# Kernel tuning notes

Hardware: AMD Instinct MI355X
Metric: run time of the kernel (lower is better)

Reference implementation:

```python
import jax, jax.numpy as jnp
import numpy as np

H = 1024        # hidden_size
V = 50257       # output_size (vocab)
L = 2048        # max_length (encoder sequence)


def setup_inputs() -> dict:
    key = jax.random.key(0)
    ks = jax.random.split(key, 10)
    s = 1.0 / np.sqrt(H)
    return {
        "input_tok": jax.random.randint(ks[0], (1,), 0, V),
        "hidden": jax.random.normal(ks[1], (2, 1, H), dtype=jnp.float32),
        "encoder_hiddens": jax.random.normal(ks[2], (L, H), dtype=jnp.float32),
        # learned parameters
        "emb": jax.random.normal(ks[3], (V, H), dtype=jnp.float32),
        "W_ih": jax.random.uniform(ks[4], (2, H, H), jnp.float32, -s, s),   # per-direction input weights
        "W_hh": jax.random.uniform(ks[5], (2, H, H), jnp.float32, -s, s),   # per-direction recurrent weights
        "b_ih": jax.random.uniform(ks[6], (2, H), jnp.float32, -s, s),
        "b_hh": jax.random.uniform(ks[7], (2, H), jnp.float32, -s, s),
        "W_out": jax.random.uniform(ks[8], (V, 4 * H), jnp.float32, -s, s),
        "b_out": jax.random.uniform(ks[9], (V,), jnp.float32, -s, s),
    }


def reference(input_tok, hidden, encoder_hiddens, emb, W_ih, W_hh, b_ih, b_hh, W_out, b_out):
    # embedding lookup -> (H,)  (dropout is identity in eval mode)
    x = emb[input_tok[0]]
    # single-step bidirectional vanilla RNN cell (both directions see the same x):
    # h' = tanh(x W_ih^T + b_ih + h0 W_hh^T + b_hh), per direction d in {fwd, bwd}
    h0 = hidden[:, 0, :]                                    # (2, H)
    h = jnp.tanh(jnp.einsum('dho,o->dh', W_ih, x) + b_ih
                 + jnp.einsum('dho,do->dh', W_hh, h0) + b_hh)  # (2, H)
    # dot-product attention per direction over encoder states (L, H)
    energy = jnp.einsum('dh,lh->dl', h, encoder_hiddens)    # (2, L)
    attn = jax.nn.softmax(energy, axis=-1)                  # (2, L)
    attn_out = jnp.einsum('dl,lh->dh', attn, encoder_hiddens)  # (2, H)
    # concat: (attn_fwd, h_fwd, attn_bwd, h_bwd) -> (1, 4H)
    concat = jnp.concatenate([attn_out[0], h[0], attn_out[1], h[1]])[None, :]
    logits = concat @ W_out.T + b_out                       # (1, V)
    output = jax.nn.log_softmax(logits, axis=1)
    return output, h[:, None, :]                            # ((1, V), (2, 1, H))
```

## Files before the change

kernel.cpp:

```cpp
#include <hip/hip_runtime.h>
#include <cmath>

#define HDIM 1024
#define LSEQ 2048
#define VOCAB 50257
#define LOGIT_BLOCKS ((VOCAB + 3) / 4)

__device__ __forceinline__ float wave_sum(float v) {
#pragma unroll
    for (int off = 32; off; off >>= 1) v += __shfl_down(v, off, 64);
    return v;
}

__device__ __forceinline__ void lse_combine(float& m, float& s, float m2, float s2) {
    float nm = fmaxf(m, m2);
    s = s * expf(m - nm) + s2 * expf(m2 - nm);
    m = nm;
}

__global__ void rnn_kernel(const int* __restrict__ tok,
                           const float* __restrict__ hidden,
                           const float* __restrict__ emb,
                           const float* __restrict__ W_ih,
                           const float* __restrict__ W_hh,
                           const float* __restrict__ b_ih,
                           const float* __restrict__ b_hh,
                           float* __restrict__ concat,
                           float* __restrict__ out_h) {
    int wave = threadIdx.x >> 6, lane = threadIdx.x & 63;
    int row = blockIdx.x * 4 + wave;
    int d = row >> 10, i = row & 1023;
    int t = tok[0];
    const float* x  = emb + (size_t)t * HDIM;
    const float* h0 = hidden + d * HDIM;
    const float* wi = W_ih + (size_t)d * HDIM * HDIM + (size_t)i * HDIM;
    const float* wh = W_hh + (size_t)d * HDIM * HDIM + (size_t)i * HDIM;
    float acc = 0.f;
#pragma unroll
    for (int p = 0; p < 4; ++p) {
        int o = p * 256 + lane * 4;
        float4 a = *(const float4*)(wi + o);
        float4 b = *(const float4*)(x + o);
        acc += a.x * b.x + a.y * b.y + a.z * b.z + a.w * b.w;
        float4 c = *(const float4*)(wh + o);
        float4 e = *(const float4*)(h0 + o);
        acc += c.x * e.x + c.y * e.y + c.z * e.z + c.w * e.w;
    }
    acc = wave_sum(acc);
    if (lane == 0) {
        float hv = tanhf(acc + b_ih[d * HDIM + i] + b_hh[d * HDIM + i]);
        concat[d * 2048 + 1024 + i] = hv;
        out_h[d * HDIM + i] = hv;
    }
}

__global__ void flash_attn_kernel(const float* __restrict__ enc,
                                  const float* __restrict__ concat,
                                  float* __restrict__ part,
                                  float* __restrict__ pm_a,
                                  float* __restrict__ ps_a) {
    __shared__ float e_sh[32];
    int b = blockIdx.x;
    int d = b >> 6, c = b & 63;
    int t = threadIdx.x, wave = t >> 6, lane = t & 63;
    int base = c * 32;
    const float* h = concat + d * 2048 + 1024;

    for (int r = 0; r < 8; ++r) {
        int ll = wave * 8 + r;
        const float* er = enc + (size_t)(base + ll) * HDIM;
        float acc = 0.f;
#pragma unroll
        for (int p = 0; p < 4; ++p) {
            int o = p * 256 + lane * 4;
            float4 a = *(const float4*)(er + o);
            float4 bb = *(const float4*)(h + o);
            acc += a.x * bb.x + a.y * bb.y + a.z * bb.z + a.w * bb.w;
        }
        acc = wave_sum(acc);
        if (lane == 0) e_sh[ll] = acc;
    }
    __syncthreads();

    float m_c = -1e30f;
#pragma unroll
    for (int l = 0; l < 32; ++l) m_c = fmaxf(m_c, e_sh[l]);
    float s_c = 0.f;
    float acc0 = 0, acc1 = 0, acc2 = 0, acc3 = 0;
    for (int l = 0; l < 32; ++l) {
        float p = expf(e_sh[l] - m_c);
        s_c += p;
        const float* row = enc + (size_t)(base + l) * HDIM;
        acc0 += p * row[t];
        acc1 += p * row[t + 256];
        acc2 += p * row[t + 512];
        acc3 += p * row[t + 768];
    }
    float* pp = part + (size_t)b * HDIM;
    pp[t] = acc0; pp[t + 256] = acc1; pp[t + 512] = acc2; pp[t + 768] = acc3;
    if (t == 0) { pm_a[b] = m_c; ps_a[b] = s_c; }
}

__global__ void attn_combine_kernel(const float* __restrict__ part,
                                    const float* __restrict__ pm_a,
                                    const float* __restrict__ ps_a,
                                    float* __restrict__ concat) {
    int idx = blockIdx.x * 256 + threadIdx.x;
    int d = idx >> 10, h = idx & 1023;
    float M = -1e30f;
    for (int c = 0; c < 64; ++c) M = fmaxf(M, pm_a[d * 64 + c]);
    float S = 0.f, acc = 0.f;
    for (int c = 0; c < 64; ++c) {
        int cb = d * 64 + c;
        float w = expf(pm_a[cb] - M);
        S += ps_a[cb] * w;
        acc += part[(size_t)cb * HDIM + h] * w;
    }
    concat[d * 2048 + h] = acc / S;
}

__global__ void logits_kernel(const float* __restrict__ W_out,
                              const float* __restrict__ b_out,
                              const float* __restrict__ concat,
                              float* __restrict__ logits,
                              float* __restrict__ pm,
                              float* __restrict__ ps) {
    __shared__ float lv[4];
    int wave = threadIdx.x >> 6, lane = threadIdx.x & 63;
    int v = blockIdx.x * 4 + wave;
    bool valid = v < VOCAB;
    int vc = valid ? v : (VOCAB - 1);
    const float* w = W_out + (size_t)vc * 4096;
    float acc = 0.f;
#pragma unroll
    for (int p = 0; p < 16; ++p) {
        int o = p * 256 + lane * 4;
        float4 a = *(const float4*)(w + o);
        float4 b = *(const float4*)(concat + o);
        acc += a.x * b.x + a.y * b.y + a.z * b.z + a.w * b.w;
    }
    acc = wave_sum(acc);
    if (lane == 0) {
        float val = acc + b_out[vc];
        if (valid) logits[v] = val;
        lv[wave] = valid ? val : -1e30f;
    }
    __syncthreads();
    if (threadIdx.x == 0) {
        float m = fmaxf(fmaxf(lv[0], lv[1]), fmaxf(lv[2], lv[3]));
        float s = 0.f;
#pragma unroll
        for (int k = 0; k < 4; ++k)
            if (lv[k] > -1e29f) s += expf(lv[k] - m);
        pm[blockIdx.x] = m;
        ps[blockIdx.x] = s;
    }
}

__global__ void out_kernel(const float* __restrict__ logits,
                           const float* __restrict__ pm,
                           const float* __restrict__ ps,
                           float* __restrict__ out) {
    __shared__ float rm[4], rs[4], Msh;
    int t = threadIdx.x, lane = t & 63, wave = t >> 6;
    float m = -1e30f, s = 0.f;
    for (int i = t; i < LOGIT_BLOCKS; i += 256) lse_combine(m, s, pm[i], ps[i]);
#pragma unroll
    for (int off = 32; off; off >>= 1) {
        float m2 = __shfl_down(m, off, 64);
        float s2 = __shfl_down(s, off, 64);
        lse_combine(m, s, m2, s2);
    }
    if (lane == 0) { rm[wave] = m; rs[wave] = s; }
    __syncthreads();
    if (t == 0) {
        float fm = rm[0], fs = rs[0];
        for (int k = 1; k < 4; ++k) lse_combine(fm, fs, rm[k], rs[k]);
        Msh = fm + logf(fs);
    }
    __syncthreads();
    float M = Msh;
    int v = blockIdx.x * 256 + t;
    if (v < VOCAB) out[v] = logits[v] - M;
}

extern "C" void kernel_launch(void* const* d_in, const int* in_sizes, int n_in,
                              void* d_out, int out_size, void* d_ws, size_t ws_size,
                              hipStream_t stream) {
    const int*   tok    = (const int*)d_in[0];
    const float* hidden = (const float*)d_in[1];
    const float* enc    = (const float*)d_in[2];
    const float* emb    = (const float*)d_in[3];
    const float* W_ih   = (const float*)d_in[4];
    const float* W_hh   = (const float*)d_in[5];
    const float* b_ih   = (const float*)d_in[6];
    const float* b_hh   = (const float*)d_in[7];
    const float* W_out  = (const float*)d_in[8];
    const float* b_out  = (const float*)d_in[9];
    float* out = (float*)d_out;

    float* ws     = (float*)d_ws;
    float* concat = ws;
    float* pm_a   = ws + 4096;
    float* ps_a   = ws + 4224;
    float* pm     = ws + 4352;
    float* ps     = ws + 16928;
    float* part   = ws + 29504;
    float* logits = ws + 29504;

    rnn_kernel<<<512, 256, 0, stream>>>(tok, hidden, emb, W_ih, W_hh, b_ih, b_hh,
                                        concat, out + VOCAB);
    flash_attn_kernel<<<128, 256, 0, stream>>>(enc, concat, part, pm_a, ps_a);
    attn_combine_kernel<<<8, 256, 0, stream>>>(part, pm_a, ps_a, concat);
    logits_kernel<<<LOGIT_BLOCKS, 256, 0, stream>>>(W_out, b_out, concat, logits, pm, ps);
    out_kernel<<<(VOCAB + 255) / 256, 256, 0, stream>>>(logits, pm, ps, out);
}
```

Before: 183.5 us.

## Split logsumexp partials into separate kernel and use nontemporal W_out loads

Removes the per-block shared-memory logsumexp reduction and __syncthreads from the logits GEMV, letting each wave write its logit and exit early. A new 128-block kernel computes the partial max and sum over all logits. The final kernel then combines only 128 partials instead of about 12.5k per block. W_out rows are read with nontemporal loads to avoid polluting the cache with the streamed 800MB matrix, at the cost of one extra kernel launch and an extra pass over the logits.

```diff
diff --git a/kernel.cpp b/kernel.cpp
--- a/kernel.cpp
+++ b/kernel.cpp
@@ -4,7 +4,8 @@
 #define HDIM 1024
 #define LSEQ 2048
 #define VOCAB 50257
-#define LOGIT_BLOCKS ((VOCAB + 3) / 4)
+
+typedef float f4 __attribute__((ext_vector_type(4)));
 
 __device__ __forceinline__ float wave_sum(float v) {
 #pragma unroll
@@ -122,38 +123,44 @@
 __global__ void logits_kernel(const float* __restrict__ W_out,
                               const float* __restrict__ b_out,
                               const float* __restrict__ concat,
-                              float* __restrict__ logits,
-                              float* __restrict__ pm,
-                              float* __restrict__ ps) {
-    __shared__ float lv[4];
+                              float* __restrict__ logits) {
     int wave = threadIdx.x >> 6, lane = threadIdx.x & 63;
     int v = blockIdx.x * 4 + wave;
-    bool valid = v < VOCAB;
-    int vc = valid ? v : (VOCAB - 1);
-    const float* w = W_out + (size_t)vc * 4096;
+    if (v >= VOCAB) return;
+    const float* w = W_out + (size_t)v * 4096;
     float acc = 0.f;
 #pragma unroll
     for (int p = 0; p < 16; ++p) {
         int o = p * 256 + lane * 4;
-        float4 a = *(const float4*)(w + o);
+        f4 a = __builtin_nontemporal_load((const f4*)(w + o));
         float4 b = *(const float4*)(concat + o);
         acc += a.x * b.x + a.y * b.y + a.z * b.z + a.w * b.w;
     }
     acc = wave_sum(acc);
-    if (lane == 0) {
-        float val = acc + b_out[vc];
-        if (valid) logits[v] = val;
-        lv[wave] = valid ? val : -1e30f;
-    }
+    if (lane == 0) logits[v] = acc + b_out[v];
+}
+
+__global__ void lse_partial_kernel(const float* __restrict__ logits,
+                                   float* __restrict__ pm,
+                                   float* __restrict__ ps) {
+    __shared__ float rm[4], rs[4];
+    int tid = blockIdx.x * 256 + threadIdx.x;
+    float m = -1e30f, s = 0.f;
+    for (int v = tid; v < VOCAB; v += 128 * 256) lse_combine(m, s, logits[v], 1.f);
+    int lane = threadIdx.x & 63, wave = threadIdx.x >> 6;
+#pragma unroll
+    for (int off = 32; off; off >>= 1) {
+        float m2 = __shfl_down(m, off, 64);
+        float s2 = __shfl_down(s, off, 64);
+        lse_combine(m, s, m2, s2);
+    }
+    if (lane == 0) { rm[wave] = m; rs[wave] = s; }
     __syncthreads();
     if (threadIdx.x == 0) {
-        float m = fmaxf(fmaxf(lv[0], lv[1]), fmaxf(lv[2], lv[3]));
-        float s = 0.f;
-#pragma unroll
-        for (int k = 0; k < 4; ++k)
-            if (lv[k] > -1e29f) s += expf(lv[k] - m);
-        pm[blockIdx.x] = m;
-        ps[blockIdx.x] = s;
+        float fm = rm[0], fs = rs[0];
+        for (int w = 1; w < 4; ++w) lse_combine(fm, fs, rm[w], rs[w]);
+        pm[blockIdx.x] = fm;
+        ps[blockIdx.x] = fs;
     }
 }
 
@@ -161,21 +168,21 @@
                            const float* __restrict__ pm,
                            const float* __restrict__ ps,
                            float* __restrict__ out) {
-    __shared__ float rm[4], rs[4], Msh;
+    __shared__ float rm[2], rs[2], Msh;
     int t = threadIdx.x, lane = t & 63, wave = t >> 6;
     float m = -1e30f, s = 0.f;
-    for (int i = t; i < LOGIT_BLOCKS; i += 256) lse_combine(m, s, pm[i], ps[i]);
+    if (t < 128) { m = pm[t]; s = ps[t]; }
 #pragma unroll
     for (int off = 32; off; off >>= 1) {
         float m2 = __shfl_down(m, off, 64);
         float s2 = __shfl_down(s, off, 64);
         lse_combine(m, s, m2, s2);
     }
-    if (lane == 0) { rm[wave] = m; rs[wave] = s; }
+    if (lane == 0 && wave < 2) { rm[wave] = m; rs[wave] = s; }
     __syncthreads();
     if (t == 0) {
         float fm = rm[0], fs = rs[0];
-        for (int k = 1; k < 4; ++k) lse_combine(fm, fs, rm[k], rs[k]);
+        lse_combine(fm, fs, rm[1], rs[1]);
         Msh = fm + logf(fs);
     }
     __syncthreads();
@@ -204,14 +211,15 @@
     float* pm_a   = ws + 4096;
     float* ps_a   = ws + 4224;
     float* pm     = ws + 4352;
-    float* ps     = ws + 16928;
-    float* part   = ws + 29504;
-    float* logits = ws + 29504;
+    float* ps     = ws + 4480;
+    float* part   = ws + 4608;
+    float* logits = ws + 4608;
 
     rnn_kernel<<<512, 256, 0, stream>>>(tok, hidden, emb, W_ih, W_hh, b_ih, b_hh,
                                         concat, out + VOCAB);
     flash_attn_kernel<<<128, 256, 0, stream>>>(enc, concat, part, pm_a, ps_a);
     attn_combine_kernel<<<8, 256, 0, stream>>>(part, pm_a, ps_a, concat);
-    logits_kernel<<<LOGIT_BLOCKS, 256, 0, stream>>>(W_out, b_out, concat, logits, pm, ps);
+    logits_kernel<<<(VOCAB + 3) / 4, 256, 0, stream>>>(W_out, b_out, concat, logits);
+    lse_partial_kernel<<<128, 256, 0, stream>>>(logits, pm, ps);
     out_kernel<<<(VOCAB + 255) / 256, 256, 0, stream>>>(logits, pm, ps, out);
 }
```

Result: faster. 154.5 us (median of 2 runs) (-15.8%).

## Compute two vocab rows per wave with nontemporal loads and move LSE to output kernel

Applied to the files above, without the earlier changes.

The logits GEMV now processes two W_out rows per wave using nontemporal loads, which halves the block count and gives each wave more loads in flight. Bias addition and the per-block max/sum partials are dropped from the logits kernel. Each output block instead recomputes the full log-sum-exp directly from the logits plus bias with an online update, and handles the last odd element separately. This removes the shared-memory sync and partial writes from the bandwidth-bound GEMV, at the cost of every output block redundantly scanning all ~50K logits.

```diff
diff --git a/kernel.cpp b/kernel.cpp
--- a/kernel.cpp
+++ b/kernel.cpp
@@ -4,7 +4,10 @@
 #define HDIM 1024
 #define LSEQ 2048
 #define VOCAB 50257
-#define LOGIT_BLOCKS ((VOCAB + 3) / 4)
+#define NPAIR ((VOCAB + 1) / 2)
+#define PAIR_BLOCKS ((NPAIR + 3) / 4)
+
+typedef float f4 __attribute__((ext_vector_type(4)));
 
 __device__ __forceinline__ float wave_sum(float v) {
 #pragma unroll
@@ -16,6 +19,11 @@
     float nm = fmaxf(m, m2);
     s = s * expf(m - nm) + s2 * expf(m2 - nm);
     m = nm;
+}
+
+__device__ __forceinline__ void lse_push(float& m, float& s, float x) {
+    if (x > m) { s = s * expf(m - x) + 1.f; m = x; }
+    else       { s += expf(x - m); }
 }
 
 __global__ void rnn_kernel(const int* __restrict__ tok,
@@ -120,51 +128,47 @@
 }
 
 __global__ void logits_kernel(const float* __restrict__ W_out,
-                              const float* __restrict__ b_out,
                               const float* __restrict__ concat,
-                              float* __restrict__ logits,
-                              float* __restrict__ pm,
-                              float* __restrict__ ps) {
-    __shared__ float lv[4];
+                              float* __restrict__ logits) {
     int wave = threadIdx.x >> 6, lane = threadIdx.x & 63;
-    int v = blockIdx.x * 4 + wave;
-    bool valid = v < VOCAB;
-    int vc = valid ? v : (VOCAB - 1);
-    const float* w = W_out + (size_t)vc * 4096;
-    float acc = 0.f;
-#pragma unroll
+    int pair = blockIdx.x * 4 + wave;
+    if (pair >= NPAIR) return;
+    int v0 = pair * 2;
+    bool v1ok = (v0 + 1) < VOCAB;
+    const float* w0 = W_out + (size_t)v0 * 4096;
+    const float* w1 = v1ok ? (w0 + 4096) : w0;
+    float acc0 = 0.f, acc1 = 0.f;
+#pragma unroll 8
     for (int p = 0; p < 16; ++p) {
         int o = p * 256 + lane * 4;
-        float4 a = *(const float4*)(w + o);
+        f4 a0 = __builtin_nontemporal_load((const f4*)(w0 + o));
+        f4 a1 = __builtin_nontemporal_load((const f4*)(w1 + o));
         float4 b = *(const float4*)(concat + o);
-        acc += a.x * b.x + a.y * b.y + a.z * b.z + a.w * b.w;
-    }
-    acc = wave_sum(acc);
+        acc0 += a0.x * b.x + a0.y * b.y + a0.z * b.z + a0.w * b.w;
+        acc1 += a1.x * b.x + a1.y * b.y + a1.z * b.z + a1.w * b.w;
+    }
+    acc0 = wave_sum(acc0);
+    acc1 = wave_sum(acc1);
     if (lane == 0) {
-        float val = acc + b_out[vc];
-        if (valid) logits[v] = val;
-        lv[wave] = valid ? val : -1e30f;
-    }
-    __syncthreads();
-    if (threadIdx.x == 0) {
-        float m = fmaxf(fmaxf(lv[0], lv[1]), fmaxf(lv[2], lv[3]));
-        float s = 0.f;
-#pragma unroll
-        for (int k = 0; k < 4; ++k)
-            if (lv[k] > -1e29f) s += expf(lv[k] - m);
-        pm[blockIdx.x] = m;
-        ps[blockIdx.x] = s;
-    }
-}
-
-__global__ void out_kernel(const float* __restrict__ logits,
-                           const float* __restrict__ pm,
-                           const float* __restrict__ ps,
-                           float* __restrict__ out) {
+        logits[v0] = acc0;
+        if (v1ok) logits[v0 + 1] = acc1;
+    }
+}
+
+__global__ void lse_out_kernel(const float* __restrict__ logits,
+                               const float* __restrict__ b_out,
+                               float* __restrict__ out) {
     __shared__ float rm[4], rs[4], Msh;
     int t = threadIdx.x, lane = t & 63, wave = t >> 6;
     float m = -1e30f, s = 0.f;
-    for (int i = t; i < LOGIT_BLOCKS; i += 256) lse_combine(m, s, pm[i], ps[i]);
+    for (int g = t; g < 12564; g += 256) {
+        float4 lv = *(const float4*)(logits + g * 4);
+        float4 bv = *(const float4*)(b_out + g * 4);
+        lse_push(m, s, lv.x + bv.x);
+        lse_push(m, s, lv.y + bv.y);
+        lse_push(m, s, lv.z + bv.z);
+        lse_push(m, s, lv.w + bv.w);
+    }
 #pragma unroll
     for (int off = 32; off; off >>= 1) {
         float m2 = __shfl_down(m, off, 64);
@@ -176,12 +180,13 @@
     if (t == 0) {
         float fm = rm[0], fs = rs[0];
         for (int k = 1; k < 4; ++k) lse_combine(fm, fs, rm[k], rs[k]);
+        lse_push(fm, fs, logits[VOCAB - 1] + b_out[VOCAB - 1]);
         Msh = fm + logf(fs);
     }
     __syncthreads();
     float M = Msh;
     int v = blockIdx.x * 256 + t;
-    if (v < VOCAB) out[v] = logits[v] - M;
+    if (v < VOCAB) out[v] = (logits[v] + b_out[v]) - M;
 }
 
 extern "C" void kernel_launch(void* const* d_in, const int* in_sizes, int n_in,
@@ -203,15 +208,13 @@
     float* concat = ws;
     float* pm_a   = ws + 4096;
     float* ps_a   = ws + 4224;
-    float* pm     = ws + 4352;
-    float* ps     = ws + 16928;
-    float* part   = ws + 29504;
-    float* logits = ws + 29504;
+    float* part   = ws + 4608;
+    float* logits = ws + 4608;
 
     rnn_kernel<<<512, 256, 0, stream>>>(tok, hidden, emb, W_ih, W_hh, b_ih, b_hh,
                                         concat, out + VOCAB);
     flash_attn_kernel<<<128, 256, 0, stream>>>(enc, concat, part, pm_a, ps_a);
     attn_combine_kernel<<<8, 256, 0, stream>>>(part, pm_a, ps_a, concat);
-    logits_kernel<<<LOGIT_BLOCKS, 256, 0, stream>>>(W_out, b_out, concat, logits, pm, ps);
-    out_kernel<<<(VOCAB + 255) / 256, 256, 0, stream>>>(logits, pm, ps, out);
-}
+    logits_kernel<<<PAIR_BLOCKS, 256, 0, stream>>>(W_out, concat, logits);
+    lse_out_kernel<<<(VOCAB + 255) / 256, 256, 0, stream>>>(logits, b_out, out);
+}
```

Result: no change. 183.8 us (+0.1%).
